# Optimization experiments

Hardware: AMD Instinct MI355X
Metric: run time of the kernel (lower is better)

Reference implementation:

```python
import jax, jax.numpy as jnp
import numpy as np

WINDOW = 16      # window_size[0]
LANDM_H = 8      # closest_square_factors(64) = (8, 8)
LANDM_W = 8
MAX_VAL = 5.0
PINV_ITERS = 6


def activ(x):
    # ExpLinearAfterThreshold: exp(clamp(x, max=5)) + relu(x - 5)
    return jnp.exp(jnp.minimum(x, MAX_VAL)) + jax.nn.relu(x - MAX_VAL)


def pool_landmarks(x):
    # x: [B, H, N, d] with N = WINDOW*WINDOW.
    B, H, N, d = x.shape
    kh, kw = WINDOW // LANDM_H, WINDOW // LANDM_W
    x = x.reshape(B, H, LANDM_H, kh, LANDM_W, kw, d)
    return x.mean(axis=(3, 5)).reshape(B, H, LANDM_H * LANDM_W, d)  # [B, H, L, d]


def moore_penrose_pinv(x, iters=PINV_ITERS):
    # x: [B, H, L, L]
    abs_x = jnp.abs(x)
    col = abs_x.sum(axis=-1)
    row = abs_x.sum(axis=-2)
    z = jnp.swapaxes(x, -1, -2) / (jnp.max(col) * jnp.max(row) + 1e-15)
    I = jnp.eye(x.shape[-1], dtype=x.dtype)
    for _ in range(iters):
        xz = x @ z
        z = 0.25 * z @ (13.0 * I - xz @ (15.0 * I - xz @ (7.0 * I - xz)))
    return z


def setup_inputs() -> dict:
    key = jax.random.key(0)
    kq, kk, kv = jax.random.split(key, 3)
    shape = (256, 16, 256, 64)  # [B_, num_heads, window^2, head_dim]
    q = jax.random.normal(kq, shape, dtype=jnp.float32)
    k = jax.random.normal(kk, shape, dtype=jnp.float32)
    v = jax.random.normal(kv, shape, dtype=jnp.float32)
    return {"q": q, "k": k, "v": v}


def reference(q, k, v):
    # q, k, v: [B, H, N, d]
    q_m = pool_landmarks(q)  # [B, H, L, d]
    k_m = pool_landmarks(k)  # [B, H, L, d]

    temp = activ(jnp.einsum('bhld,bhmd->bhlm', q_m, k_m))   # [B, H, L, L]
    pinv = moore_penrose_pinv(temp, PINV_ITERS)              # [B, H, L, L]

    # kernel(q_m, k) @ [v | 1]  -> [B, H, L, d+1]
    v1 = jnp.concatenate([v, jnp.ones_like(v[..., :1])], axis=-1)
    kv = jnp.einsum('bhln,bhne->bhle', activ(jnp.einsum('bhld,bhnd->bhln', q_m, k)), v1)

    # kernel(q, k_m) @ pinv @ kv  -> [B, H, N, d+1]
    qk = activ(jnp.einsum('bhnd,bhld->bhnl', q, k_m))        # [B, H, N, L]
    prod = jnp.einsum('bhnl,bhle->bhne', qk @ pinv, kv)

    return prod[..., :-1] / (prod[..., -1:] + 1e-12)
```

## Files before the change

kernel.cpp:

```cpp
#include <hip/hip_runtime.h>
#include <math.h>


#define G_TOT 4096
#define TPB_R 256
#define TPB_M 1024
typedef _Float16 f16;
typedef __attribute__((ext_vector_type(2))) _Float16 f16x2;
typedef __attribute__((ext_vector_type(4))) _Float16 f16x4;
typedef __attribute__((ext_vector_type(8))) _Float16 f16x8;
typedef __attribute__((ext_vector_type(4))) float f32x4;
typedef __attribute__((ext_vector_type(16))) float f32x16;

#define NPLANES 16
#define SMEM_BYTES (NPLANES * 4096 * 2 + 256)

#define LSCALE 2048.0f
#define LINV   (1.0f / 2048.0f)
#define ZS     1024.0f
#define ZINV   (1.0f / 1024.0f)

struct HL { f16 h, l; };
__device__ __forceinline__ HL split2(float v) {
    HL r;
    r.h = (f16)v;
    r.l = (f16)((v - (float)r.h) * LSCALE);
    return r;
}
__device__ __forceinline__ float join2(f16 h, f16 l) {
    return (float)h + (float)l * LINV;
}
__device__ __forceinline__ int swi(int r, int c) {
    return (r << 6) + (c ^ ((r & 7) << 3));
}
__device__ __forceinline__ float activ_f(float x) {
    return __expf(fminf(x, 5.0f)) + fmaxf(x - 5.0f, 0.0f);
}
__device__ __forceinline__ float activ_r(float x) {
    return expf(fminf(x, 5.0f)) + fmaxf(x - 5.0f, 0.0f);
}
__device__ __forceinline__ void split_w(f16* Ph, f16* Pl, int r, int c, float v) {
    HL s = split2(v);
    const int o = swi(r, c);
    Ph[o] = s.h;
    Pl[o] = s.l;
}
__device__ __forceinline__ f16x2 mk2(f16 a, f16 b) { f16x2 r; r[0]=a; r[1]=b; return r; }
__device__ __forceinline__ f16x4 mk4(f16 a, f16 b, f16 c, f16 d) { f16x4 r; r[0]=a;r[1]=b;r[2]=c;r[3]=d; return r; }
__device__ __forceinline__ f32x4 z4() { f32x4 z = {0.f,0.f,0.f,0.f}; return z; }
__device__ __forceinline__ f32x16 z16() {
    f32x16 z;
#pragma unroll
    for (int i = 0; i < 16; ++i) z[i] = 0.f;
    return z;
}

struct Frag { f16x8 h[2], l[2]; };

__device__ __forceinline__ Frag ld_frag(const f16* __restrict__ Ph,
                                        const f16* __restrict__ Pl,
                                        int row, int kg) {
    Frag f;
    const int base = row << 6, x = (row & 7) << 3;
#pragma unroll
    for (int s = 0; s < 2; ++s) {
        const int o = base + ((((s << 5) + (kg << 3))) ^ x);
        f.h[s] = *(const f16x8*)(Ph + o);
        f.l[s] = *(const f16x8*)(Pl + o);
    }
    return f;
}

__device__ __forceinline__ f32x4 mm16_rr(const Frag& A, const Frag& B, f32x4 acc) {
    f32x4 ax = z4();
#pragma unroll
    for (int s = 0; s < 2; ++s) {
        acc = __builtin_amdgcn_mfma_f32_16x16x32_f16(A.h[s], B.h[s], acc, 0, 0, 0);
        ax  = __builtin_amdgcn_mfma_f32_16x16x32_f16(A.h[s], B.l[s], ax, 0, 0, 0);
        ax  = __builtin_amdgcn_mfma_f32_16x16x32_f16(A.l[s], B.h[s], ax, 0, 0, 0);
    }
    acc += ax * LINV;
    return acc;
}

__device__ __forceinline__ void wfrag_rm(f16* Ph, f16* Pl, int Rb, int C, const float* v) {
#pragma unroll
    for (int m = 0; m < 4; ++m) split_w(Ph, Pl, Rb + m, C, v[m]);
}
__device__ __forceinline__ void wfrag_t(f16* Ph, f16* Pl, int Rb, int C, const float* v) {
    const int o = swi(C, Rb);
    HL s0 = split2(v[0]), s1 = split2(v[1]), s2 = split2(v[2]), s3 = split2(v[3]);
    *(f16x4*)(Ph + o) = mk4(s0.h, s1.h, s2.h, s3.h);
    *(f16x4*)(Pl + o) = mk4(s0.l, s1.l, s2.l, s3.l);
}

__device__ __forceinline__ void wr_rm(float4 vv, f16* Ph, f16* Pl, int t) {
    const int r = t >> 4, c4 = (t & 15) << 2;
    const int o = swi(r, c4);
    HL s0 = split2(vv.x), s1 = split2(vv.y), s2 = split2(vv.z), s3 = split2(vv.w);
    *(f16x4*)(Ph + o) = mk4(s0.h, s1.h, s2.h, s3.h);
    *(f16x4*)(Pl + o) = mk4(s0.l, s1.l, s2.l, s3.l);
}
__device__ __forceinline__ void ld_vt(const float* __restrict__ src, int t,
                                      float2& va, float2& vb) {
    const int n0 = (t >> 5) << 1, e0 = (t & 31) << 1;
    va = *(const float2*)(src + (size_t)n0 * 64 + e0);
    vb = *(const float2*)(src + (size_t)(n0 + 1) * 64 + e0);
}
__device__ __forceinline__ void wr_vt(float2 va, float2 vb, f16* Ph, f16* Pl, int t) {
    const int n0 = (t >> 5) << 1, e0 = (t & 31) << 1;
    HL ax = split2(va.x), ay = split2(va.y), bx = split2(vb.x), by = split2(vb.y);
    const int o0 = swi(e0, n0), o1 = swi(e0 + 1, n0);
    *(f16x2*)(Ph + o0) = mk2(ax.h, bx.h);
    *(f16x2*)(Pl + o0) = mk2(ax.l, bx.l);
    *(f16x2*)(Ph + o1) = mk2(ay.h, by.h);
    *(f16x2*)(Pl + o1) = mk2(ay.l, by.l);
}
__device__ __forceinline__ void pool_global1024(const float* __restrict__ src,
                                                f16* Ph, f16* Pl, int t) {
    const int L = t >> 4, d0 = (t & 15) << 2;
    const int nb = ((L >> 3) << 5) + ((L & 7) << 1);
    const float* p = src + (size_t)nb * 64 + d0;
    float4 a = *(const float4*)p;
    float4 b = *(const float4*)(p + 64);
    float4 c = *(const float4*)(p + 1024);
    float4 d = *(const float4*)(p + 1088);
    HL s0 = split2(0.25f * (a.x + b.x + c.x + d.x));
    HL s1 = split2(0.25f * (a.y + b.y + c.y + d.y));
    HL s2 = split2(0.25f * (a.z + b.z + c.z + d.z));
    HL s3 = split2(0.25f * (a.w + b.w + c.w + d.w));
    const int o = swi(L, d0);
    *(f16x4*)(Ph + o) = mk4(s0.h, s1.h, s2.h, s3.h);
    *(f16x4*)(Pl + o) = mk4(s0.l, s1.l, s2.l, s3.l);
}
__device__ __forceinline__ void pool_lds512(const f16* Kh, const f16* Kl,
                                            f16* Ph, f16* Pl, int t, int tt) {
    const int ll = t >> 5, d0 = (t & 31) << 1;
    const int rb = ((ll >> 3) << 5) + ((ll & 7) << 1);
    float s0 = 0.f, s1 = 0.f;
#pragma unroll
    for (int rr = 0; rr < 4; ++rr) {
        const int r = rb + (rr & 1) + ((rr >> 1) << 4);
        const int o = swi(r, d0);
        f16x2 h = *(const f16x2*)(Kh + o);
        f16x2 l = *(const f16x2*)(Kl + o);
        s0 += join2(h[0], l[0]);
        s1 += join2(h[1], l[1]);
    }
    const int L = (tt << 4) + ll;
    HL p0 = split2(0.25f * s0), p1 = split2(0.25f * s1);
    const int o = swi(L, d0);
    *(f16x2*)(Ph + o) = mk2(p0.h, p1.h);
    *(f16x2*)(Pl + o) = mk2(p0.l, p1.l);
}

__device__ __forceinline__ f32x16 mm64q(const f16* __restrict__ Ah, const f16* __restrict__ Al,
                                        const f16* __restrict__ Bh, const f16* __restrict__ Bl,
                                        int lane, int wr, int wc, f32x16 acc) {
    const int cl = lane & 31, hh = lane >> 5;
    const int ar = (wr << 5) + cl, br = (wc << 5) + cl;
    const int abase = ar << 6, axor = (ar & 7) << 3;
    const int bbase = br << 6, bxor = (br & 7) << 3;
    f32x16 ax1 = z16();
    f32x16 ax2 = z16();
#pragma unroll
    for (int ks = 0; ks < 4; ++ks) {
        const int k0 = (ks << 4) + (hh << 3);
        const int ao = abase + (k0 ^ axor);
        const int bo = bbase + (k0 ^ bxor);
        f16x8 a_h = *(const f16x8*)(Ah + ao);
        f16x8 a_l = *(const f16x8*)(Al + ao);
        f16x8 b_h = *(const f16x8*)(Bh + bo);
        f16x8 b_l = *(const f16x8*)(Bl + bo);
        acc = __builtin_amdgcn_mfma_f32_32x32x16_f16(a_h, b_h, acc, 0, 0, 0);
        ax1 = __builtin_amdgcn_mfma_f32_32x32x16_f16(a_h, b_l, ax1, 0, 0, 0);
        ax2 = __builtin_amdgcn_mfma_f32_32x32x16_f16(a_l, b_h, ax2, 0, 0, 0);
    }
    acc += (ax1 + ax2) * LINV;
    return acc;
}
__device__ __forceinline__ void pool_global_r(const float* __restrict__ src,
                                              f16* Ph, f16* Pl, int t) {
    const int ll = t >> 4, d0 = (t & 15) << 2;
    const int rb = ((ll >> 3) << 5) + ((ll & 7) << 1);
#pragma unroll
    for (int tt = 0; tt < 4; ++tt) {
        const float* p = src + (size_t)((tt << 6) + rb) * 64 + d0;
        float4 a = *(const float4*)p;
        float4 b = *(const float4*)(p + 64);
        float4 c = *(const float4*)(p + 1024);
        float4 d = *(const float4*)(p + 1088);
        const int L = (tt << 4) + ll;
        split_w(Ph, Pl, L, d0 + 0, 0.25f * (a.x + b.x + c.x + d.x));
        split_w(Ph, Pl, L, d0 + 1, 0.25f * (a.y + b.y + c.y + d.y));
        split_w(Ph, Pl, L, d0 + 2, 0.25f * (a.z + b.z + c.z + d.z));
        split_w(Ph, Pl, L, d0 + 3, 0.25f * (a.w + b.w + c.w + d.w));
    }
}

#define WAVE_SUM32(v)            \
    v += __shfl_xor(v, 1);       \
    v += __shfl_xor(v, 2);       \
    v += __shfl_xor(v, 4);       \
    v += __shfl_xor(v, 8);       \
    v += __shfl_xor(v, 16);

__global__ void k_init(float* ws) {
    if (threadIdx.x < 2) ws[threadIdx.x] = 0.0f;
}

__global__ __launch_bounds__(TPB_R) void k_reduce(const float* __restrict__ q,
                                                  const float* __restrict__ k,
                                                  float* __restrict__ ws) {
    __shared__ f16 pls[4 * 4096];
    __shared__ float rowS[64], colS[64];
    const int t = threadIdx.x, g = blockIdx.x;
    const int lane = t & 63, wv = t >> 6, wr = wv >> 1, wc = wv & 1;
    const int cl = lane & 31, hh = lane >> 5;
    if (t < 64) rowS[t] = 0.f;
    else if (t < 128) colS[t - 64] = 0.f;
    pool_global_r(q + (size_t)g * 16384, pls, pls + 4096, t);
    pool_global_r(k + (size_t)g * 16384, pls + 8192, pls + 12288, t);
    __syncthreads();
    f32x16 a = mm64q(pls, pls + 4096, pls + 8192, pls + 12288, lane, wr, wc, z16());
    float colp = 0.f;
#pragma unroll
    for (int m = 0; m < 16; ++m) {
        float x = activ_r(a[m]);
        const int R = (wr << 5) + (m & 3) + ((m >> 2) << 3) + (hh << 2);
        float vs = x;
        WAVE_SUM32(vs)
        if (cl == 0) atomicAdd(&rowS[R], vs);
        colp += x;
    }
    colp += __shfl_xor(colp, 32);
    if (hh == 0) atomicAdd(&colS[(wc << 5) + cl], colp);
    __syncthreads();
    if (t < 64) {
        float vmx = rowS[t];
        for (int off = 1; off < 64; off <<= 1) vmx = fmaxf(vmx, __shfl_xor(vmx, off));
        if (t == 0) atomicMax((int*)ws, __float_as_int(vmx));
    } else if (t < 128) {
        float vmx = colS[t - 64];
        for (int off = 1; off < 64; off <<= 1) vmx = fmaxf(vmx, __shfl_xor(vmx, off));
        if (t == 64) atomicMax(((int*)ws) + 1, __float_as_int(vmx));
    }
}

__global__ __launch_bounds__(TPB_M, 4) void k_main(const float* __restrict__ q,
                                                   const float* __restrict__ k,
                                                   const float* __restrict__ v,
                                                   const float* __restrict__ ws,
                                                   float* __restrict__ out) {
    extern __shared__ f16 smu[];
    f16* kv1h = smu + NPLANES * 4096;
    f16* kv1l = kv1h + 64;
    const int t = threadIdx.x, g = blockIdx.x;
    const int lane = t & 63, w = t >> 6;
    const int ti = w & 3, tj = w >> 2;
    const int fr = lane & 15, kg = lane >> 4;
    const int arow = (ti << 4) + fr;
    const int brow = (tj << 4) + fr;
    const int C = brow;
    const int Rb = (ti << 4) + (kg << 2);
    const float* Gq = q + (size_t)g * 16384;
    const float* Gk = k + (size_t)g * 16384;
    const float* Gv = v + (size_t)g * 16384;
    float* og = out + (size_t)g * 16384;

    f16* Xh  = smu +  0 * 4096; f16* Xl  = smu +  1 * 4096;
    f16* SAh = smu +  2 * 4096; f16* SAl = smu +  3 * 4096;
    f16* SBh = smu +  4 * 4096; f16* SBl = smu +  5 * 4096;
    f16* KMh = smu +  6 * 4096; f16* KMl = smu +  7 * 4096;
    f16* SCh = smu +  8 * 4096; f16* SCl = smu +  9 * 4096;
    f16* KVh = smu + 10 * 4096; f16* KVl = smu + 11 * 4096;
    f16* Z0rh= smu + 12 * 4096; f16* Z0rl= smu + 13 * 4096;
    f16* Z0th= smu + 14 * 4096; f16* Z0tl= smu + 15 * 4096;

    Frag fOnes;
    {
        f16x8 one8, zer8;
#pragma unroll
        for (int i = 0; i < 8; ++i) { one8[i] = (f16)1.0f; zer8[i] = (f16)0.0f; }
        fOnes.h[0] = one8; fOnes.h[1] = one8;
        fOnes.l[0] = zer8; fOnes.l[1] = zer8;
    }

    pool_global1024(Gq, Z0rh, Z0rl, t);
    {
        float4 kreg = *(const float4*)(Gk + (size_t)t * 4);
        float2 va, vb; ld_vt(Gv, t, va, vb);
        wr_rm(kreg, SAh, SAl, t);
        wr_vt(va, vb, SBh, SBl, t);
    }
    __syncthreads();

    Frag fQM = ld_frag(Z0rh, Z0rl, arow, kg);

    f32x4 kva = z4();
    f32x4 kva1 = z4();
    for (int tt = 0; tt < 4; ++tt) {
        f16* vch = (tt & 1) ? Xh : SBh;  f16* vcl = (tt & 1) ? Xl : SBl;
        f16* vnh = (tt & 1) ? SBh : Xh;  f16* vnl = (tt & 1) ? SBl : Xl;
        float4 kregN; float2 vaN, vbN;
        if (tt < 3) {
            kregN = *(const float4*)(Gk + (size_t)(tt + 1) * 4096 + (size_t)t * 4);
            ld_vt(Gv + (size_t)(tt + 1) * 4096, t, vaN, vbN);
        }
        if (t < 512) pool_lds512(SAh, SAl, KMh, KMl, t, tt);
        {
            Frag bK = ld_frag(SAh, SAl, brow, kg);
            f32x4 s = mm16_rr(fQM, bK, z4());
            float sv[4];
#pragma unroll
            for (int m = 0; m < 4; ++m) sv[m] = activ_f(s[m]);
            wfrag_rm(SCh, SCl, Rb, C, sv);
        }
        if (tt < 3) wr_vt(vaN, vbN, vnh, vnl, t);
        __syncthreads();
        {
            Frag aS = ld_frag(SCh, SCl, arow, kg);
            Frag bV = ld_frag(vch, vcl, brow, kg);
            kva  = mm16_rr(aS, bV, kva);
            kva1 = mm16_rr(aS, fOnes, kva1);
        }
        if (tt < 3) wr_rm(kregN, SAh, SAl, t);
        __syncthreads();
    }

    {
        float kvv[4] = {kva[0], kva[1], kva[2], kva[3]};
        wfrag_t(KVh, KVl, Rb, C, kvv);
        Frag fKMb = ld_frag(KMh, KMl, brow, kg);
        f32x4 x0 = mm16_rr(fQM, fKMb, z4());
        const float scale = ZS / (ws[0] * ws[1] + 1e-15f);
        float xv[4], zv[4];
#pragma unroll
        for (int m = 0; m < 4; ++m) { xv[m] = activ_f(x0[m]); zv[m] = xv[m] * scale; }
        wfrag_rm(Xh, Xl, Rb, C, xv);
        wfrag_t (Z0rh, Z0rl, Rb, C, zv);
        wfrag_rm(Z0th, Z0tl, Rb, C, zv);
        if (tj == 0 && fr == 0) {
#pragma unroll
            for (int m = 0; m < 4; ++m) {
                HL s = split2(kva1[m]);
                kv1h[Rb + m] = s.h;
                kv1l[Rb + m] = s.l;
            }
        }
    }
    __syncthreads();

    Frag fX = ld_frag(Xh, Xl, arow, kg);
#pragma unroll
    for (int it = 0; it < 6; ++it) {
        Frag bz = ld_frag(Z0th, Z0tl, brow, kg);
        f32x4 a1 = mm16_rr(fX, bz, z4());
        float t1k[4];
#pragma unroll
        for (int m = 0; m < 4; ++m) t1k[m] = a1[m] * ZINV;
        wfrag_rm(SAh, SAl, Rb, C, t1k);
        wfrag_t (SCh, SCl, Rb, C, t1k);
        __syncthreads();
        Frag aM  = ld_frag(SAh, SAl, arow, kg);
        Frag bMt = ld_frag(SCh, SCl, brow, kg);
        f32x4 pP = mm16_rr(aM, bMt, z4());
        Frag aZ  = ld_frag(Z0rh, Z0rl, arow, kg);
        f32x4 wS = mm16_rr(aZ, bMt, z4());
        float opv[4], wv[4];
#pragma unroll
        for (int m = 0; m < 4; ++m) { opv[m] = 7.f * t1k[m] - pP[m]; wv[m] = wS[m]; }
        wfrag_t (Xh, Xl, Rb, C, opv);
        wfrag_rm(SBh, SBl, Rb, C, wv);
        __syncthreads();
        Frag aW  = ld_frag(SBh, SBl, arow, kg);
        Frag bOP = ld_frag(Xh, Xl, brow, kg);
        f32x4 yS = mm16_rr(aW, bOP, z4());
        float zk[4];
#pragma unroll
        for (int m = 0; m < 4; ++m) {
            const int o = swi(Rb + m, C);
            const float zs = join2(Z0rh[o], Z0rl[o]);
            zk[m] = 0.25f * (13.f * zs - 15.f * wv[m] + yS[m]);
        }
        wfrag_rm(Z0rh, Z0rl, Rb, C, zk);
        wfrag_t (Z0th, Z0tl, Rb, C, zk);
        __syncthreads();
    }

    float4 qp0, qp1, qp2, qp3;
#define LOAD_Q(tt_)                                                              \
    {                                                                            \
        const float* rp = Gq + (size_t)(((tt_) << 6) + arow) * 64 + (kg << 3);   \
        qp0 = *(const float4*)(rp);      qp1 = *(const float4*)(rp + 4);         \
        qp2 = *(const float4*)(rp + 32); qp3 = *(const float4*)(rp + 36);        \
    }
#define BUILD_AQ(aQ_)                                                                          \
    {                                                                                          \
        HL s0 = split2(qp0.x), s1 = split2(qp0.y), s2 = split2(qp0.z), s3 = split2(qp0.w);     \
        HL s4 = split2(qp1.x), s5 = split2(qp1.y), s6 = split2(qp1.z), s7 = split2(qp1.w);     \
        f16x8 h, l;                                                                            \
        h[0]=s0.h; h[1]=s1.h; h[2]=s2.h; h[3]=s3.h; h[4]=s4.h; h[5]=s5.h; h[6]=s6.h; h[7]=s7.h;\
        l[0]=s0.l; l[1]=s1.l; l[2]=s2.l; l[3]=s3.l; l[4]=s4.l; l[5]=s5.l; l[6]=s6.l; l[7]=s7.l;\
        aQ_.h[0] = h; aQ_.l[0] = l;                                                            \
        HL t0 = split2(qp2.x), t1 = split2(qp2.y), t2 = split2(qp2.z), t3 = split2(qp2.w);     \
        HL t4 = split2(qp3.x), t5 = split2(qp3.y), t6 = split2(qp3.z), t7 = split2(qp3.w);     \
        f16x8 h2, l2;                                                                          \
        h2[0]=t0.h; h2[1]=t1.h; h2[2]=t2.h; h2[3]=t3.h; h2[4]=t4.h; h2[5]=t5.h; h2[6]=t6.h; h2[7]=t7.h; \
        l2[0]=t0.l; l2[1]=t1.l; l2[2]=t2.l; l2[3]=t3.l; l2[4]=t4.l; l2[5]=t5.l; l2[6]=t6.l; l2[7]=t7.l; \
        aQ_.h[1] = h2; aQ_.l[1] = l2;                                                          \
    }
#define DO_QK(dsth, dstl)                                             \
    {                                                                 \
        Frag aQ; BUILD_AQ(aQ)                                         \
        Frag bKM = ld_frag(KMh, KMl, brow, kg);                       \
        f32x4 q0 = mm16_rr(aQ, bKM, z4());                            \
        float qv[4];                                                  \
        _Pragma("unroll")                                             \
        for (int m = 0; m < 4; ++m) qv[m] = activ_f(q0[m]);           \
        wfrag_rm(dsth, dstl, Rb, C, qv);                              \
    }
#define DO_W(srch, srcl, dsth, dstl)                                  \
    {                                                                 \
        Frag aK = ld_frag(srch, srcl, arow, kg);                      \
        Frag bZt = ld_frag(Z0th, Z0tl, brow, kg);                     \
        f32x4 w0 = mm16_rr(aK, bZt, z4());                            \
        float wv2[4];                                                 \
        _Pragma("unroll")                                             \
        for (int m = 0; m < 4; ++m) wv2[m] = w0[m] * ZINV;            \
        wfrag_rm(dsth, dstl, Rb, C, wv2);                             \
    }
#define DO_PROD(srch, srcl, tt_)                                      \
    {                                                                 \
        Frag aW2 = ld_frag(srch, srcl, arow, kg);                     \
        Frag bKV = ld_frag(KVh, KVl, brow, kg);                       \
        f32x4 p0 = mm16_rr(aW2, bKV, z4());                           \
        Frag fk;                                                      \
        _Pragma("unroll")                                             \
        for (int s = 0; s < 2; ++s) {                                 \
            const int o = (s << 5) + (kg << 3);                       \
            fk.h[s] = *(const f16x8*)(kv1h + o);                      \
            fk.l[s] = *(const f16x8*)(kv1l + o);                      \
        }                                                             \
        f32x4 d4 = mm16_rr(aW2, fk, z4());                            \
        _Pragma("unroll")                                             \
        for (int m = 0; m < 4; ++m) {                                 \
            const int R = Rb + m;                                     \
            og[(size_t)(((tt_) << 6) + R) * 64 + C] = p0[m] / (d4[m] + 1e-12f); \
        }                                                             \
    }

    LOAD_Q(0)
    DO_QK(SCh, SCl)
    LOAD_Q(1)
    __syncthreads();
    DO_W(SCh, SCl, SBh, SBl)
    DO_QK(SAh, SAl)
    LOAD_Q(2)
    __syncthreads();
    DO_PROD(SBh, SBl, 0)
    DO_W(SAh, SAl, Xh, Xl)
    DO_QK(SCh, SCl)
    LOAD_Q(3)
    __syncthreads();
    DO_PROD(Xh, Xl, 1)
    DO_W(SCh, SCl, SBh, SBl)
    DO_QK(SAh, SAl)
    __syncthreads();
    DO_PROD(SBh, SBl, 2)
    DO_W(SAh, SAl, Xh, Xl)
    __syncthreads();
    DO_PROD(Xh, Xl, 3)
#undef LOAD_Q
#undef BUILD_AQ
#undef DO_QK
#undef DO_W
#undef DO_PROD
}

extern "C" void kernel_launch(void* const* d_in, const int* in_sizes, int n_in,
                              void* d_out, int out_size, void* d_ws, size_t ws_size,
                              hipStream_t stream) {
    const float* q = (const float*)d_in[0];
    const float* k = (const float*)d_in[1];
    const float* v = (const float*)d_in[2];
    float* out = (float*)d_out;
    float* ws  = (float*)d_ws;
    (void)in_sizes; (void)n_in; (void)out_size; (void)ws_size;

    hipFuncSetAttribute((const void*)k_main,
                        hipFuncAttributeMaxDynamicSharedMemorySize, SMEM_BYTES);

    k_init<<<1, 64, 0, stream>>>(ws);
    k_reduce<<<G_TOT, TPB_R, 0, stream>>>(q, k, ws);
    k_main<<<G_TOT, TPB_M, SMEM_BYTES, stream>>>(q, k, v, ws, out);
}
```

Before: 758.7 us.

## Use 32x32x16 MFMA tiles for pinv iterations on a subset of warps

Rewrites the 64x64 Moore-Penrose iteration loop so that only 4 or 8 wavefronts compute it with 32x32x16 MFMA tiles instead of every wave doing 16x16 tiles. Warps 0-3 keep X fragments in registers and handle the xz and P products, while warps 4-7 keep z in registers across iterations and handle the W and Y products, which splits the two independent products across wave groups. This is meant to cut LDS fragment reloads and MFMA instruction count, at the cost of idle waves during the loop and higher register pressure.

```diff
diff --git a/kernel.cpp b/kernel.cpp
--- a/kernel.cpp
+++ b/kernel.cpp
@@ -56,6 +56,7 @@
 }
 
 struct Frag { f16x8 h[2], l[2]; };
+struct Frag32 { f16x8 h, l; };
 
 __device__ __forceinline__ Frag ld_frag(const f16* __restrict__ Ph,
                                         const f16* __restrict__ Pl,
@@ -71,6 +72,18 @@
     return f;
 }
 
+__device__ __forceinline__ Frag32 ld_frag32(const f16* __restrict__ Ph,
+                                            const f16* __restrict__ Pl,
+                                            int rowbase, int lane, int ks) {
+    const int r = rowbase + (lane & 31);
+    const int k0 = (ks << 4) + ((lane >> 5) << 3);
+    const int o = (r << 6) + (k0 ^ ((r & 7) << 3));
+    Frag32 f;
+    f.h = *(const f16x8*)(Ph + o);
+    f.l = *(const f16x8*)(Pl + o);
+    return f;
+}
+
 __device__ __forceinline__ f32x4 mm16_rr(const Frag& A, const Frag& B, f32x4 acc) {
     f32x4 ax = z4();
 #pragma unroll
@@ -78,6 +91,36 @@
         acc = __builtin_amdgcn_mfma_f32_16x16x32_f16(A.h[s], B.h[s], acc, 0, 0, 0);
         ax  = __builtin_amdgcn_mfma_f32_16x16x32_f16(A.h[s], B.l[s], ax, 0, 0, 0);
         ax  = __builtin_amdgcn_mfma_f32_16x16x32_f16(A.l[s], B.h[s], ax, 0, 0, 0);
+    }
+    acc += ax * LINV;
+    return acc;
+}
+
+__device__ __forceinline__ f32x16 mm32(const f16* __restrict__ Ah, const f16* __restrict__ Al, int arb,
+                                       const f16* __restrict__ Bh, const f16* __restrict__ Bl, int brb,
+                                       int lane, f32x16 acc) {
+    f32x16 ax = z16();
+#pragma unroll
+    for (int ks = 0; ks < 4; ++ks) {
+        Frag32 A = ld_frag32(Ah, Al, arb, lane, ks);
+        Frag32 B = ld_frag32(Bh, Bl, brb, lane, ks);
+        acc = __builtin_amdgcn_mfma_f32_32x32x16_f16(A.h, B.h, acc, 0, 0, 0);
+        ax  = __builtin_amdgcn_mfma_f32_32x32x16_f16(A.h, B.l, ax, 0, 0, 0);
+        ax  = __builtin_amdgcn_mfma_f32_32x32x16_f16(A.l, B.h, ax, 0, 0, 0);
+    }
+    acc += ax * LINV;
+    return acc;
+}
+__device__ __forceinline__ f32x16 mm32_ca(const Frag32* __restrict__ Af,
+                                          const f16* __restrict__ Bh, const f16* __restrict__ Bl, int brb,
+                                          int lane, f32x16 acc) {
+    f32x16 ax = z16();
+#pragma unroll
+    for (int ks = 0; ks < 4; ++ks) {
+        Frag32 B = ld_frag32(Bh, Bl, brb, lane, ks);
+        acc = __builtin_amdgcn_mfma_f32_32x32x16_f16(Af[ks].h, B.h, acc, 0, 0, 0);
+        ax  = __builtin_amdgcn_mfma_f32_32x32x16_f16(Af[ks].h, B.l, ax, 0, 0, 0);
+        ax  = __builtin_amdgcn_mfma_f32_32x32x16_f16(Af[ks].l, B.h, ax, 0, 0, 0);
     }
     acc += ax * LINV;
     return acc;
@@ -92,6 +135,26 @@
     HL s0 = split2(v[0]), s1 = split2(v[1]), s2 = split2(v[2]), s3 = split2(v[3]);
     *(f16x4*)(Ph + o) = mk4(s0.h, s1.h, s2.h, s3.h);
     *(f16x4*)(Pl + o) = mk4(s0.l, s1.l, s2.l, s3.l);
+}
+__device__ __forceinline__ void wfrag32_rm(f16* Ph, f16* Pl, int rb, int cb, int lane, const float* v) {
+    const int C = cb + (lane & 31), hh4 = ((lane >> 5) << 2);
+#pragma unroll
+    for (int m = 0; m < 16; ++m) {
+        const int R = rb + (m & 3) + ((m >> 2) << 3) + hh4;
+        split_w(Ph, Pl, R, C, v[m]);
+    }
+}
+__device__ __forceinline__ void wfrag32_t(f16* Ph, f16* Pl, int rb, int cb, int lane, const float* v) {
+    const int C = cb + (lane & 31), hh4 = ((lane >> 5) << 2);
+#pragma unroll
+    for (int g = 0; g < 4; ++g) {
+        const int R0 = rb + (g << 3) + hh4;
+        const int o = swi(C, R0);
+        HL s0 = split2(v[(g << 2)]), s1 = split2(v[(g << 2) + 1]);
+        HL s2 = split2(v[(g << 2) + 2]), s3 = split2(v[(g << 2) + 3]);
+        *(f16x4*)(Ph + o) = mk4(s0.h, s1.h, s2.h, s3.h);
+        *(f16x4*)(Pl + o) = mk4(s0.l, s1.l, s2.l, s3.l);
+    }
 }
 
 __device__ __forceinline__ void wr_rm(float4 vv, f16* Ph, f16* Pl, int t) {
@@ -351,40 +414,56 @@
     }
     __syncthreads();
 
-    Frag fX = ld_frag(Xh, Xl, arow, kg);
-#pragma unroll
+    const int idx2 = w & 3;
+    const int rb32 = (idx2 >> 1) << 5;
+    const int cb32 = (idx2 & 1) << 5;
+    const int cl31 = lane & 31, hh4 = ((lane >> 5) << 2);
+    Frag32 fX32[4];
+    float zs[16], wvv[16], t1k32[16];
+    if (w < 4) {
+#pragma unroll
+        for (int ks = 0; ks < 4; ++ks) fX32[ks] = ld_frag32(Xh, Xl, rb32, lane, ks);
+    } else if (w < 8) {
+#pragma unroll
+        for (int m = 0; m < 16; ++m) {
+            const int R = rb32 + (m & 3) + ((m >> 2) << 3) + hh4;
+            const int o = swi(R, cb32 + cl31);
+            zs[m] = join2(Z0rh[o], Z0rl[o]);
+        }
+    }
     for (int it = 0; it < 6; ++it) {
-        Frag bz = ld_frag(Z0th, Z0tl, brow, kg);
-        f32x4 a1 = mm16_rr(fX, bz, z4());
-        float t1k[4];
-#pragma unroll
-        for (int m = 0; m < 4; ++m) t1k[m] = a1[m] * ZINV;
-        wfrag_rm(SAh, SAl, Rb, C, t1k);
-        wfrag_t (SCh, SCl, Rb, C, t1k);
+        if (w < 4) {
+            f32x16 a1 = mm32_ca(fX32, Z0th, Z0tl, cb32, lane, z16());
+#pragma unroll
+            for (int m = 0; m < 16; ++m) t1k32[m] = a1[m] * ZINV;
+            wfrag32_rm(SAh, SAl, rb32, cb32, lane, t1k32);
+            wfrag32_t (SCh, SCl, rb32, cb32, lane, t1k32);
+        }
         __syncthreads();
-        Frag aM  = ld_frag(SAh, SAl, arow, kg);
-        Frag bMt = ld_frag(SCh, SCl, brow, kg);
-        f32x4 pP = mm16_rr(aM, bMt, z4());
-        Frag aZ  = ld_frag(Z0rh, Z0rl, arow, kg);
-        f32x4 wS = mm16_rr(aZ, bMt, z4());
-        float opv[4], wv[4];
-#pragma unroll
-        for (int m = 0; m < 4; ++m) { opv[m] = 7.f * t1k[m] - pP[m]; wv[m] = wS[m]; }
-        wfrag_t (Xh, Xl, Rb, C, opv);
-        wfrag_rm(SBh, SBl, Rb, C, wv);
+        if (w < 4) {
+            f32x16 pP = mm32(SAh, SAl, rb32, SCh, SCl, cb32, lane, z16());
+            float opv[16];
+#pragma unroll
+            for (int m = 0; m < 16; ++m) opv[m] = 7.f * t1k32[m] - pP[m];
+            wfrag32_t(Xh, Xl, rb32, cb32, lane, opv);
+        } else if (w < 8) {
+            f32x16 wS = mm32(Z0rh, Z0rl, rb32, SCh, SCl, cb32, lane, z16());
+#pragma unroll
+            for (int m = 0; m < 16; ++m) wvv[m] = wS[m];
+            wfrag32_rm(SBh, SBl, rb32, cb32, lane, wvv);
+        }
         __syncthreads();
-        Frag aW  = ld_frag(SBh, SBl, arow, kg);
-        Frag bOP = ld_frag(Xh, Xl, brow, kg);
-        f32x4 yS = mm16_rr(aW, bOP, z4());
-        float zk[4];
-#pragma unroll
-        for (int m = 0; m < 4; ++m) {
-            const int o = swi(Rb + m, C);
-            const float zs = join2(Z0rh[o], Z0rl[o]);
-            zk[m] = 0.25f * (13.f * zs - 15.f * wv[m] + yS[m]);
-        }
-        wfrag_rm(Z0rh, Z0rl, Rb, C, zk);
-        wfrag_t (Z0th, Z0tl, Rb, C, zk);
+        if (w >= 4 && w < 8) {
+            f32x16 yS = mm32(SBh, SBl, rb32, Xh, Xl, cb32, lane, z16());
+            float zk[16];
+#pragma unroll
+            for (int m = 0; m < 16; ++m) {
+                zk[m] = 0.25f * (13.f * zs[m] - 15.f * wvv[m] + yS[m]);
+                zs[m] = zk[m];
+            }
+            wfrag32_rm(Z0rh, Z0rl, rb32, cb32, lane, zk);
+            wfrag32_t (Z0th, Z0tl, rb32, cb32, lane, zk);
+        }
         __syncthreads();
     }
 
```

Result: slower. 2.105 ms (+177.5%).
